# Performance work log

Hardware: AMD Instinct MI355X
Metric: run time of the kernel (lower is better)

Reference implementation:

```python
import jax, jax.numpy as jnp
import numpy as np

N_NODES = 50000
N_RAND_EDGES = 800000
NEG_SLOPE = 0.2


def setup_inputs() -> dict:
    key = jax.random.key(0)
    ks = jax.random.split(key, 10)
    src_r = jax.random.randint(ks[0], (N_RAND_EDGES,), 0, N_NODES, dtype=jnp.int32)
    dst_r = jax.random.randint(ks[1], (N_RAND_EDGES,), 0, N_NODES, dtype=jnp.int32)
    loops = jnp.arange(N_NODES, dtype=jnp.int32)
    src = jnp.concatenate([src_r, loops])  # [E] with self-loops -> no empty softmax segment
    dst = jnp.concatenate([dst_r, loops])
    return {
        "x": jax.random.normal(ks[2], (N_NODES, 256), dtype=jnp.float32),
        "src": src,
        "dst": dst,
        "W0": jax.random.normal(ks[3], (256, 4 * 64), dtype=jnp.float32) * 0.05,
        "al0": jax.random.normal(ks[4], (4, 64), dtype=jnp.float32) * 0.05,
        "ar0": jax.random.normal(ks[5], (4, 64), dtype=jnp.float32) * 0.05,
        "W1": jax.random.normal(ks[6], (256, 1 * 32), dtype=jnp.float32) * 0.05,
        "al1": jax.random.normal(ks[7], (1, 32), dtype=jnp.float32) * 0.05,
        "ar1": jax.random.normal(ks[8], (1, 32), dtype=jnp.float32) * 0.05,
        "Wres": jax.random.normal(ks[9], (256, 32), dtype=jnp.float32) * 0.05,
    }


def gat_conv(x, src, dst, W, al, ar, Wres, activation):
    """DGL-style GATConv. x: [N, F]; W: [F, H*D]; al/ar: [H, D]."""
    N = x.shape[0]
    H, D = al.shape
    feat = (x @ W).reshape(N, H, D)                       # [N,H,D]
    el = jnp.sum(feat * al, axis=-1)                      # [N,H]
    er = jnp.sum(feat * ar, axis=-1)                      # [N,H]
    e = jax.nn.leaky_relu(el[src] + er[dst], NEG_SLOPE)   # [E,H]
    # edge softmax over incoming edges of each dst node
    emax = jax.ops.segment_max(e, dst, num_segments=N)    # [N,H]
    ex = jnp.exp(e - emax[dst])
    denom = jax.ops.segment_sum(ex, dst, num_segments=N)  # [N,H]
    alpha = ex / denom[dst]                               # [E,H]
    msg = feat[src] * alpha[:, :, None]                   # [E,H,D]
    out = jax.ops.segment_sum(msg, dst, num_segments=N)   # [N,H,D]
    if Wres is not None:
        out = out + (x @ Wres).reshape(N, -1, D)          # residual (broadcast over heads)
    if activation is not None:
        out = activation(out)
    return out


def reference(x, src, dst, W0, al0, ar0, W1, al1, ar1, Wres):
    N = x.shape[0]
    h = gat_conv(x, src, dst, W0, al0, ar0, None, jax.nn.elu)  # [N,4,64]
    h = h.reshape(N, -1)                                       # flatten(1) -> [N,256]
    out = gat_conv(h, src, dst, W1, al1, ar1, Wres, None)      # [N,1,32]
    logits = out.mean(axis=1)                                  # [N,32]
    return logits
```

## Files before the change

kernel.cpp:

```cpp
#include <hip/hip_runtime.h>
#include <math.h>

#define NEG_SLOPE 0.2f

typedef __attribute__((ext_vector_type(8))) short short8;
typedef __attribute__((ext_vector_type(4))) float f32x4;
typedef unsigned int uintx2 __attribute__((ext_vector_type(2)));
typedef unsigned int uintx4 __attribute__((ext_vector_type(4)));

__device__ __forceinline__ float leaky(float x) { return x > 0.f ? x : NEG_SLOPE * x; }
__device__ __forceinline__ unsigned enc(float f) {
    unsigned u = __float_as_uint(f);
    return (u & 0x80000000u) ? ~u : (u | 0x80000000u);
}
__device__ __forceinline__ float dec(unsigned e) {
    return (e & 0x80000000u) ? __uint_as_float(e ^ 0x80000000u) : __uint_as_float(~e);
}
__device__ __forceinline__ unsigned bf16u(float f) {
    unsigned u = __float_as_uint(f);
    return (u + 0x7fffu + ((u >> 16) & 1u)) >> 16;
}
__device__ __forceinline__ float blo(unsigned u) { return __uint_as_float(u << 16); }
__device__ __forceinline__ float bhi(unsigned u) { return __uint_as_float(u & 0xffff0000u); }

__global__ __launch_bounds__(256) void prep_kernel(const float* __restrict__ W0,
                                                   unsigned short* __restrict__ W0P,
                                                   const float* __restrict__ W1,
                                                   const float* __restrict__ Wres,
                                                   unsigned short* __restrict__ Bt1,
                                                   const int* __restrict__ dst,
                                                   int* __restrict__ deg, int E) {
    int b = blockIdx.x, tid = threadIdx.x;
    if (b < 256) {
        int n = b, k = tid;
        W0P[(k >> 5) * 8192 + n * 32 + (k & 31)] = (unsigned short)bf16u(W0[k * 256 + n]);
    } else if (b < 320) {
        int n = b - 256, k = tid;
        float v = (n < 32) ? W1[k * 32 + n] : Wres[k * 32 + (n - 32)];
        Bt1[n * 256 + k] = (unsigned short)bf16u(v);
    } else {
        int e = (b - 320) * 256 + tid;
        if (e < E) atomicAdd(&deg[dst[e]], 1);
    }
}

__global__ __launch_bounds__(256) void gemm0_all(const float* __restrict__ x,
                                                 const unsigned short* __restrict__ W0P,
                                                 unsigned short* __restrict__ featS,
                                                 float* __restrict__ el0, float* __restrict__ er0,
                                                 const float* __restrict__ al,
                                                 const float* __restrict__ ar,
                                                 unsigned* __restrict__ gmax, int M) {
    __shared__ unsigned short As[64 * 40];
    __shared__ unsigned short Bs[256 * 40];
    __shared__ __align__(16) unsigned short tile[64 * 72];
    __shared__ float sEl[4][64], sEr[4][64];
    const int K = 256;
    int tid = threadIdx.x, lane = tid & 63, wv = tid >> 6;
    int m0 = blockIdx.x * 64;
    int wm = (wv >> 1) * 32, wn = (wv & 1) * 32;
    f32x4 acc[4][2][2] = {};
    int arow = tid >> 2, apart = tid & 3;
    bool avalid = (m0 + arow) < M;
    const float* Ap = x + (size_t)min(m0 + arow, M - 1) * K + apart * 8;
    const float4 z4 = make_float4(0.f, 0.f, 0.f, 0.f);

    uint4 apReg;
    {
        float4 a0 = avalid ? *(const float4*)Ap : z4;
        float4 a1 = avalid ? *(const float4*)(Ap + 4) : z4;
        apReg.x = bf16u(a0.x) | (bf16u(a0.y) << 16);
        apReg.y = bf16u(a0.z) | (bf16u(a0.w) << 16);
        apReg.z = bf16u(a1.x) | (bf16u(a1.y) << 16);
        apReg.w = bf16u(a1.z) | (bf16u(a1.w) << 16);
    }
    uint4 b[4];
#pragma unroll
    for (int p = 0; p < 4; ++p) b[p] = *(const uint4*)(W0P + (p * 256 + tid) * 8);

    for (int k0 = 0; k0 < K; k0 += 32) {
        *(uint4*)&As[arow * 40 + apart * 8] = apReg;
#pragma unroll
        for (int p = 0; p < 4; ++p) {
            int q = p * 256 + tid;
            *(uint4*)&Bs[(q >> 2) * 40 + (q & 3) * 8] = b[p];
        }
        __syncthreads();
        if (k0 + 32 < K) {
            float4 a0 = avalid ? *(const float4*)(Ap + k0 + 32) : z4;
            float4 a1 = avalid ? *(const float4*)(Ap + k0 + 36) : z4;
            apReg.x = bf16u(a0.x) | (bf16u(a0.y) << 16);
            apReg.y = bf16u(a0.z) | (bf16u(a0.w) << 16);
            apReg.z = bf16u(a1.x) | (bf16u(a1.y) << 16);
            apReg.w = bf16u(a1.z) | (bf16u(a1.w) << 16);
            const unsigned short* slab = W0P + ((k0 >> 5) + 1) * 8192;
#pragma unroll
            for (int p = 0; p < 4; ++p) b[p] = *(const uint4*)(slab + (p * 256 + tid) * 8);
        }
        short8 af[2];
#pragma unroll
        for (int i = 0; i < 2; ++i)
            af[i] = *(const short8*)&As[(wm + i * 16 + (lane & 15)) * 40 + (lane >> 4) * 8];
#pragma unroll
        for (int y = 0; y < 4; ++y) {
            short8 bf[2];
#pragma unroll
            for (int j = 0; j < 2; ++j)
                bf[j] = *(const short8*)&Bs[(y * 64 + wn + j * 16 + (lane & 15)) * 40 + (lane >> 4) * 8];
#pragma unroll
            for (int i = 0; i < 2; ++i)
#pragma unroll
                for (int j = 0; j < 2; ++j)
                    acc[y][i][j] = __builtin_amdgcn_mfma_f32_16x16x32_bf16(af[i], bf[j], acc[y][i][j], 0, 0, 0);
        }
        __syncthreads();
    }

    size_t N32 = (size_t)M * 32;
#pragma unroll
    for (int y = 0; y < 4; ++y) {
#pragma unroll
        for (int i = 0; i < 2; ++i)
#pragma unroll
            for (int j = 0; j < 2; ++j)
#pragma unroll
                for (int r = 0; r < 4; ++r)
                    tile[(wm + i * 16 + (lane >> 4) * 4 + r) * 72 + wn + j * 16 + (lane & 15)] =
                        (unsigned short)bf16u(acc[y][i][j][r]);
        __syncthreads();
#pragma unroll
        for (int u = tid; u < 512; u += 256) {
            int ch = u >> 8, node = (u >> 2) & 63, part = u & 3;
            int row = m0 + node;
            if (row < M) {
                uint4 v = *(const uint4*)&tile[node * 72 + ch * 32 + part * 8];
                *(uint4*)&featS[(size_t)(2 * y + ch) * N32 + (size_t)row * 32 + part * 8] = v;
            }
        }
        {
            int row = tid >> 2, qr = tid & 3;
            float pe = 0.f, pr = 0.f;
            for (int k2 = 0; k2 < 16; ++k2) {
                int c = qr * 16 + k2;
                float f = __uint_as_float((unsigned)tile[row * 72 + c] << 16);
                pe += f * al[y * 64 + c];
                pr += f * ar[y * 64 + c];
            }
            pe += __shfl_xor(pe, 1); pe += __shfl_xor(pe, 2);
            pr += __shfl_xor(pr, 1); pr += __shfl_xor(pr, 2);
            if (qr == 0) {
                bool vv = (m0 + row) < M;
                if (vv) {
                    el0[(m0 + row) * 4 + y] = pe;
                    er0[(m0 + row) * 4 + y] = pr;
                }
                sEl[y][row] = vv ? pe : -1e30f;
                sEr[y][row] = vv ? pr : -1e30f;
            }
        }
        __syncthreads();
    }
    {
        float m1 = sEl[wv][lane];
        float m2 = sEr[wv][lane];
#pragma unroll
        for (int o = 1; o <= 32; o <<= 1) {
            m1 = fmaxf(m1, __shfl_xor(m1, o));
            m2 = fmaxf(m2, __shfl_xor(m2, o));
        }
        if (lane == 0) atomicMax(&gmax[wv], enc(m1));
        if (lane == 1) atomicMax(&gmax[4 + wv], enc(m2));
    }
}

__global__ __launch_bounds__(256) void gemm1_fused(const unsigned short* __restrict__ hbS,
                                                   const unsigned short* __restrict__ Bt,
                                                   float* __restrict__ fcat,
                                                   unsigned short* __restrict__ fg16,
                                                   float* __restrict__ el1, float* __restrict__ er1,
                                                   const float* __restrict__ al,
                                                   const float* __restrict__ ar,
                                                   unsigned* __restrict__ gmax, int M) {
    __shared__ unsigned short As[64 * 40];
    __shared__ unsigned short Bs[64 * 40];
    __shared__ __align__(16) float tileF[64 * 68];
    __shared__ float sEl[64], sEr[64];
    const int K = 256;
    int tid = threadIdx.x, lane = tid & 63, wv = tid >> 6;
    int m0 = blockIdx.x * 64;
    int wm = (wv >> 1) * 32, wn = (wv & 1) * 32;
    f32x4 acc[2][2] = {};
    int srow = tid >> 2, scol = (tid & 3) * 8;
    bool avalid = (m0 + srow) < M;
    size_t arow = (size_t)min(m0 + srow, M - 1);
    size_t N32 = (size_t)M * 32;
    const unsigned short* Bp = Bt + (size_t)srow * K + scol;

    for (int k0 = 0; k0 < K; k0 += 32) {
        const unsigned short* Ap = hbS + (size_t)(k0 >> 5) * N32 + arow * 32 + scol;
        uint4 av = avalid ? *(const uint4*)Ap : make_uint4(0, 0, 0, 0);
        float4 bv = *(const float4*)(Bp + k0);
        *(uint4*)&As[srow * 40 + scol] = av;
        *(float4*)&Bs[srow * 40 + scol] = bv;
        __syncthreads();
        short8 af[2], bf[2];
#pragma unroll
        for (int i = 0; i < 2; ++i) {
            af[i] = *(const short8*)&As[(wm + i * 16 + (lane & 15)) * 40 + (lane >> 4) * 8];
            bf[i] = *(const short8*)&Bs[(wn + i * 16 + (lane & 15)) * 40 + (lane >> 4) * 8];
        }
#pragma unroll
        for (int i = 0; i < 2; ++i)
#pragma unroll
            for (int j = 0; j < 2; ++j)
                acc[i][j] = __builtin_amdgcn_mfma_f32_16x16x32_bf16(af[i], bf[j], acc[i][j], 0, 0, 0);
        __syncthreads();
    }
#pragma unroll
    for (int i = 0; i < 2; ++i)
#pragma unroll
        for (int j = 0; j < 2; ++j)
#pragma unroll
            for (int r = 0; r < 4; ++r)
                tileF[(wm + i * 16 + (lane >> 4) * 4 + r) * 68 + wn + j * 16 + (lane & 15)] =
                    acc[i][j][r];
    __syncthreads();
#pragma unroll
    for (int u = tid; u < 1024; u += 256) {
        int node = u >> 4, part = u & 15;
        int row = m0 + node;
        if (row < M)
            *(uint4*)&fcat[(size_t)row * 64 + part * 4] = *(const uint4*)&tileF[node * 68 + part * 4];
    }
#pragma unroll
    for (int u = tid; u < 1024; u += 256) {
        int node = u >> 4, part = u & 15;
        int row = m0 + node;
        if (row < M) {
            float f0 = tileF[node * 68 + part * 2];
            float f1 = tileF[node * 68 + part * 2 + 1];
            ((unsigned*)fg16)[(size_t)row * 16 + part] = bf16u(f0) | (bf16u(f1) << 16);
        }
    }
    {
        int row = tid >> 2, qr = tid & 3;
        float pe = 0.f, pr = 0.f;
        for (int k = 0; k < 8; ++k) {
            int c = qr * 8 + k;
            float f = tileF[row * 68 + c];
            pe += f * al[c];
            pr += f * ar[c];
        }
        pe += __shfl_xor(pe, 1); pe += __shfl_xor(pe, 2);
        pr += __shfl_xor(pr, 1); pr += __shfl_xor(pr, 2);
        if (qr == 0) {
            bool vv = (m0 + row) < M;
            if (vv) {
                el1[m0 + row] = pe;
                er1[m0 + row] = pr;
            }
            sEl[row] = vv ? pe : -1e30f;
            sEr[row] = vv ? pr : -1e30f;
        }
    }
    __syncthreads();
    if (tid < 64) {
        float m = sEl[tid];
#pragma unroll
        for (int o = 1; o <= 32; o <<= 1) m = fmaxf(m, __shfl_xor(m, o));
        if (tid == 0) atomicMax(&gmax[8], enc(m));
    } else if (tid < 128) {
        float m = sEr[tid - 64];
#pragma unroll
        for (int o = 1; o <= 32; o <<= 1) m = fmaxf(m, __shfl_xor(m, o));
        if (tid == 64) atomicMax(&gmax[9], enc(m));
    }
}

__global__ __launch_bounds__(256) void scanA(const int* __restrict__ deg, int* __restrict__ bsum, int N) {
    int i = blockIdx.x * 256 + threadIdx.x;
    int v = (i < N) ? deg[i] : 0;
#pragma unroll
    for (int o = 32; o > 0; o >>= 1) v += __shfl_xor(v, o);
    __shared__ int s[4];
    if ((threadIdx.x & 63) == 0) s[threadIdx.x >> 6] = v;
    __syncthreads();
    if (threadIdx.x == 0) bsum[blockIdx.x] = s[0] + s[1] + s[2] + s[3];
}

__global__ __launch_bounds__(256) void scanB(const int* __restrict__ bsum, int* __restrict__ bpre, int nb) {
    __shared__ int s[256];
    int t = threadIdx.x;
    int v = (t < nb) ? bsum[t] : 0;
    s[t] = v;
    __syncthreads();
    for (int o = 1; o < 256; o <<= 1) {
        int x = (t >= o) ? s[t - o] : 0;
        __syncthreads();
        s[t] += x;
        __syncthreads();
    }
    if (t < nb) bpre[t] = s[t] - v;
}

__global__ __launch_bounds__(256) void scanC(const int* __restrict__ deg, const int* __restrict__ bpre,
                                             int* __restrict__ off, int N) {
    int b = blockIdx.x, t = threadIdx.x;
    int i = b * 256 + t;
    int v = (i < N) ? deg[i] : 0;
    __shared__ int s[256];
    s[t] = v;
    __syncthreads();
    for (int o = 1; o < 256; o <<= 1) {
        int x = (t >= o) ? s[t - o] : 0;
        __syncthreads();
        s[t] += x;
        __syncthreads();
    }
    int incl = s[t];
    int base = bpre[b];
    if (i < N) off[i] = base + incl - v;
    if (i == N - 1) off[N] = base + incl;
}

__global__ void scatter_kernel(const int* __restrict__ src, const int* __restrict__ dst,
                               const int* __restrict__ off, int* __restrict__ cursor,
                               int* __restrict__ csr_src, int E) {
    int e = blockIdx.x * 256 + threadIdx.x;
    if (e < E) {
        int d = dst[e];
        int pos = atomicAdd(&cursor[d], 1);
        csr_src[off[d] + pos] = src[e];
    }
}

__global__ __launch_bounds__(256) void w0norm(const float* __restrict__ el,
                                              const float* __restrict__ er,
                                              const unsigned* __restrict__ gmax,
                                              const int* __restrict__ off,
                                              const int* __restrict__ csr_src,
                                              unsigned* __restrict__ pk0,
                                              float* __restrict__ dinv0, int N, int E) {
    int tid = threadIdx.x, lane = tid & 63, wv = tid >> 6;
    int grp = lane >> 4, j = lane & 15;
    float C0 = leaky(dec(gmax[0]) + dec(gmax[4]));
    float C1 = leaky(dec(gmax[1]) + dec(gmax[5]));
    float C2 = leaky(dec(gmax[2]) + dec(gmax[6]));
    float C3 = leaky(dec(gmax[3]) + dec(gmax[7]));
    int n = blockIdx.x * 16 + wv * 4 + grp;
    if (n >= N) return;
    int base = off[n], deg = off[n + 1] - base;
    float4 ern = *(const float4*)&er[n * 4];
    float d0 = 0.f, d1 = 0.f, d2 = 0.f, d3 = 0.f;
    for (int j0 = 0; j0 < deg; j0 += 16) {
        int jj = j0 + j;
        if (jj < deg) {
            int idx = base + jj;
            int s = csr_src[idx];
            float4 e4 = *(const float4*)&el[s * 4];
            unsigned b0 = bf16u(__expf(leaky(e4.x + ern.x) - C0));
            unsigned b1 = bf16u(__expf(leaky(e4.y + ern.y) - C1));
            unsigned b2 = bf16u(__expf(leaky(e4.z + ern.z) - C2));
            unsigned b3 = bf16u(__expf(leaky(e4.w + ern.w) - C3));
            unsigned sh = (unsigned)s << 16;
            pk0[idx] = sh | b0;
            pk0[E + idx] = sh | b1;
            pk0[2 * E + idx] = sh | b2;
            pk0[3 * E + idx] = sh | b3;
            d0 += __uint_as_float(b0 << 16);
            d1 += __uint_as_float(b1 << 16);
            d2 += __uint_as_float(b2 << 16);
            d3 += __uint_as_float(b3 << 16);
        }
    }
#pragma unroll
    for (int o = 1; o <= 8; o <<= 1) {
        d0 += __shfl_xor(d0, o);
        d1 += __shfl_xor(d1, o);
        d2 += __shfl_xor(d2, o);
        d3 += __shfl_xor(d3, o);
    }
    if (j == 0) {
        float4 iv = make_float4(1.f / d0, 1.f / d1, 1.f / d2, 1.f / d3);
        *(float4*)&dinv0[n * 4] = iv;
    }
}

__global__ __launch_bounds__(256) void w1norm(const float* __restrict__ el,
                                              const float* __restrict__ er,
                                              const unsigned* __restrict__ gmax,
                                              const int* __restrict__ off,
                                              const int* __restrict__ csr_src,
                                              unsigned* __restrict__ pk1,
                                              float* __restrict__ dinv1, int N) {
    int tid = threadIdx.x, lane = tid & 63, wv = tid >> 6;
    float C = leaky(dec(gmax[8]) + dec(gmax[9]));
    int n = blockIdx.x * 4 + wv;
    if (n >= N) return;
    int base = off[n], deg = off[n + 1] - base;
    float ern = er[n];
    float den = 0.f;
    for (int j0 = 0; j0 < deg; j0 += 64) {
        int jj = j0 + lane;
        if (jj < deg) {
            int idx = base + jj;
            int s = csr_src[idx];
            unsigned b = bf16u(__expf(leaky(el[s] + ern) - C));
            pk1[idx] = ((unsigned)s << 16) | b;
            den += __uint_as_float(b << 16);
        }
    }
#pragma unroll
    for (int o = 1; o <= 32; o <<= 1) den += __shfl_xor(den, o);
    if (lane == 0) dinv1[n] = 1.f / den;
}

__global__ __launch_bounds__(256) void agg0_kernel(const unsigned short* __restrict__ featS,
                                                   const unsigned* __restrict__ pk0,
                                                   const float* __restrict__ dinv0,
                                                   const int* __restrict__ off,
                                                   unsigned short* __restrict__ hbS, int N, int E) {
    int tid = threadIdx.x;
    int c = blockIdx.x & 7, h = c >> 1;
    int gblk = blockIdx.x >> 3, G = gridDim.x >> 3;
    int grp = tid >> 2, ld = tid & 3;
    size_t N32 = (size_t)N * 32;
    const char* Fb = (const char*)(featS + (size_t)c * N32) + ld * 16;
    const unsigned* PH = pk0 + (size_t)h * E;
    for (int n = gblk * 64 + grp; n < N; n += G * 64) {
        int base = off[n], deg = off[n + 1] - base;
        float a0 = 0.f, a1 = 0.f, a2 = 0.f, a3 = 0.f;
        float a4 = 0.f, a5 = 0.f, a6 = 0.f, a7 = 0.f;
        const unsigned* P = PH + base;
        int j = 0;
        for (; j + 4 <= deg; j += 4) {
            unsigned p0 = P[j], p1 = P[j + 1], p2 = P[j + 2], p3 = P[j + 3];
            uintx4 u0 = *(const uintx4*)(Fb + (size_t)(p0 >> 16) * 64);
            uintx4 u1 = *(const uintx4*)(Fb + (size_t)(p1 >> 16) * 64);
            uintx4 u2 = *(const uintx4*)(Fb + (size_t)(p2 >> 16) * 64);
            uintx4 u3 = *(const uintx4*)(Fb + (size_t)(p3 >> 16) * 64);
            float w0 = blo(p0), w1 = blo(p1), w2 = blo(p2), w3 = blo(p3);
            a0 += w0 * blo(u0.x); a1 += w0 * bhi(u0.x);
            a2 += w0 * blo(u0.y); a3 += w0 * bhi(u0.y);
            a4 += w0 * blo(u0.z); a5 += w0 * bhi(u0.z);
            a6 += w0 * blo(u0.w); a7 += w0 * bhi(u0.w);
            a0 += w1 * blo(u1.x); a1 += w1 * bhi(u1.x);
            a2 += w1 * blo(u1.y); a3 += w1 * bhi(u1.y);
            a4 += w1 * blo(u1.z); a5 += w1 * bhi(u1.z);
            a6 += w1 * blo(u1.w); a7 += w1 * bhi(u1.w);
            a0 += w2 * blo(u2.x); a1 += w2 * bhi(u2.x);
            a2 += w2 * blo(u2.y); a3 += w2 * bhi(u2.y);
            a4 += w2 * blo(u2.z); a5 += w2 * bhi(u2.z);
            a6 += w2 * blo(u2.w); a7 += w2 * bhi(u2.w);
            a0 += w3 * blo(u3.x); a1 += w3 * bhi(u3.x);
            a2 += w3 * blo(u3.y); a3 += w3 * bhi(u3.y);
            a4 += w3 * blo(u3.z); a5 += w3 * bhi(u3.z);
            a6 += w3 * blo(u3.w); a7 += w3 * bhi(u3.w);
        }
        for (; j < deg; ++j) {
            unsigned p = P[j];
            float w = blo(p);
            uintx4 u = *(const uintx4*)(Fb + (size_t)(p >> 16) * 64);
            a0 += w * blo(u.x); a1 += w * bhi(u.x);
            a2 += w * blo(u.y); a3 += w * bhi(u.y);
            a4 += w * blo(u.z); a5 += w * bhi(u.z);
            a6 += w * blo(u.w); a7 += w * bhi(u.w);
        }
        float inv = dinv0[n * 4 + h];
        float v0 = a0 * inv, v1 = a1 * inv, v2 = a2 * inv, v3 = a3 * inv;
        float v4 = a4 * inv, v5 = a5 * inv, v6 = a6 * inv, v7 = a7 * inv;
        v0 = v0 > 0.f ? v0 : (__expf(v0) - 1.f);
        v1 = v1 > 0.f ? v1 : (__expf(v1) - 1.f);
        v2 = v2 > 0.f ? v2 : (__expf(v2) - 1.f);
        v3 = v3 > 0.f ? v3 : (__expf(v3) - 1.f);
        v4 = v4 > 0.f ? v4 : (__expf(v4) - 1.f);
        v5 = v5 > 0.f ? v5 : (__expf(v5) - 1.f);
        v6 = v6 > 0.f ? v6 : (__expf(v6) - 1.f);
        v7 = v7 > 0.f ? v7 : (__expf(v7) - 1.f);
        uintx4 o;
        o.x = bf16u(v0) | (bf16u(v1) << 16);
        o.y = bf16u(v2) | (bf16u(v3) << 16);
        o.z = bf16u(v4) | (bf16u(v5) << 16);
        o.w = bf16u(v6) | (bf16u(v7) << 16);
        __builtin_nontemporal_store(o, (uintx4*)&hbS[(size_t)c * N32 + (size_t)n * 32 + ld * 8]);
    }
}

__global__ __launch_bounds__(256) void agg1_kernel(const float* __restrict__ fcat,
                                                   const unsigned short* __restrict__ fg16,
                                                   const unsigned* __restrict__ pk1,
                                                   const float* __restrict__ dinv1,
                                                   const int* __restrict__ off,
                                                   float* __restrict__ out, int N) {
    int tid = threadIdx.x;
    int grp = tid >> 3, ld = tid & 7;
    const char* Fb = (const char*)fg16 + ld * 8;
    for (int n = blockIdx.x * 32 + grp; n < N; n += gridDim.x * 32) {
        int base = off[n], deg = off[n + 1] - base;
        float a0 = 0.f, a1 = 0.f, a2 = 0.f, a3 = 0.f;
        const unsigned* P = pk1 + base;
        int j = 0;
        for (; j + 4 <= deg; j += 4) {
            unsigned p0 = P[j], p1 = P[j + 1], p2 = P[j + 2], p3 = P[j + 3];
            uintx2 u0 = *(const uintx2*)(Fb + (size_t)(p0 >> 16) * 64);
            uintx2 u1 = *(const uintx2*)(Fb + (size_t)(p1 >> 16) * 64);
            uintx2 u2 = *(const uintx2*)(Fb + (size_t)(p2 >> 16) * 64);
            uintx2 u3 = *(const uintx2*)(Fb + (size_t)(p3 >> 16) * 64);
            float w0 = blo(p0), w1 = blo(p1), w2 = blo(p2), w3 = blo(p3);
            a0 += w0 * blo(u0.x); a1 += w0 * bhi(u0.x);
            a2 += w0 * blo(u0.y); a3 += w0 * bhi(u0.y);
            a0 += w1 * blo(u1.x); a1 += w1 * bhi(u1.x);
            a2 += w1 * blo(u1.y); a3 += w1 * bhi(u1.y);
            a0 += w2 * blo(u2.x); a1 += w2 * bhi(u2.x);
            a2 += w2 * blo(u2.y); a3 += w2 * bhi(u2.y);
            a0 += w3 * blo(u3.x); a1 += w3 * bhi(u3.x);
            a2 += w3 * blo(u3.y); a3 += w3 * bhi(u3.y);
        }
        for (; j < deg; ++j) {
            unsigned p = P[j];
            float w = blo(p);
            uintx2 u = *(const uintx2*)(Fb + (size_t)(p >> 16) * 64);
            a0 += w * blo(u.x); a1 += w * bhi(u.x);
            a2 += w * blo(u.y); a3 += w * bhi(u.y);
        }
        float inv = dinv1[n];
        f32x4 res = *(const f32x4*)&fcat[(size_t)n * 64 + 32 + ld * 4];
        f32x4 o;
        o.x = a0 * inv + res.x;
        o.y = a1 * inv + res.y;
        o.z = a2 * inv + res.z;
        o.w = a3 * inv + res.w;
        __builtin_nontemporal_store(o, (f32x4*)&out[(size_t)n * 32 + ld * 4]);
    }
}

extern "C" void kernel_launch(void* const* d_in, const int* in_sizes, int n_in,
                              void* d_out, int out_size, void* d_ws, size_t ws_size,
                              hipStream_t stream) {
    const float* x    = (const float*)d_in[0];
    const int*   src  = (const int*)d_in[1];
    const int*   dst  = (const int*)d_in[2];
    const float* W0   = (const float*)d_in[3];
    const float* al0  = (const float*)d_in[4];
    const float* ar0  = (const float*)d_in[5];
    const float* W1   = (const float*)d_in[6];
    const float* al1  = (const float*)d_in[7];
    const float* ar1  = (const float*)d_in[8];
    const float* Wres = (const float*)d_in[9];
    float* out = (float*)d_out;

    const int N = in_sizes[0] / 256;
    const int E = in_sizes[1];

    unsigned short* hbS   = (unsigned short*)d_ws;
    unsigned short* featS = hbS + (size_t)N * 256;
    unsigned short* W0P   = featS + (size_t)N * 256;
    unsigned short* Bt1   = W0P + 256 * 256;
    unsigned short* fg16  = Bt1 + 64 * 256;
    float* fcat  = (float*)(fg16 + (size_t)N * 32);
    float* el0   = fcat + (size_t)N * 64;
    float* er0   = el0 + (size_t)N * 4;
    float* el1   = er0 + (size_t)N * 4;
    float* er1   = el1 + N;
    float* dinv0 = er1 + N;
    float* dinv1 = dinv0 + (size_t)N * 4;
    unsigned* pk0 = (unsigned*)(dinv1 + N);
    unsigned* pk1 = pk0 + (size_t)E * 4;
    int*   deg    = (int*)(pk1 + E);
    int*   cursor = deg + N;
    unsigned* gmax = (unsigned*)(cursor + N);
    int*   offs  = (int*)(gmax + 16);
    int*   bsum  = offs + N + 1;
    int*   bpre  = bsum + 256;
    int*   csr_src = bpre + 256;

    const int nb = (N + 255) / 256;
    const int eb = (E + 255) / 256;
    const int mb = (N + 63) / 64;

    hipMemsetAsync(deg, 0, (size_t)(2 * N + 16) * sizeof(int), stream);

    prep_kernel<<<320 + eb, 256, 0, stream>>>(W0, W0P, W1, Wres, Bt1, dst, deg, E);

    scanA<<<nb, 256, 0, stream>>>(deg, bsum, N);
    scanB<<<1, 256, 0, stream>>>(bsum, bpre, nb);
    scanC<<<nb, 256, 0, stream>>>(deg, bpre, offs, N);
    scatter_kernel<<<eb, 256, 0, stream>>>(src, dst, offs, cursor, csr_src, E);

    gemm0_all<<<mb, 256, 0, stream>>>(x, W0P, featS, el0, er0, al0, ar0, gmax, N);
    w0norm<<<(N + 15) / 16, 256, 0, stream>>>(el0, er0, gmax, offs, csr_src, pk0, dinv0, N, E);
    {
        int G = (N + 63) / 64;
        agg0_kernel<<<G * 8, 256, 0, stream>>>(featS, pk0, dinv0, offs, hbS, N, E);
    }

    gemm1_fused<<<mb, 256, 0, stream>>>(hbS, Bt1, fcat, fg16, el1, er1, al1, ar1, gmax, N);
    w1norm<<<(N + 3) / 4, 256, 0, stream>>>(el1, er1, gmax, offs, csr_src, pk1, dinv1, N);
    {
        int G = (N + 31) / 32;
        agg1_kernel<<<G, 256, 0, stream>>>(fcat, fg16, pk1, dinv1, offs, out, N);
    }
}
```

Measured before the change: 303.6 us.

## Shrink gemm0 tile to 32 rows, one head per wave, register epilogue

The first-layer GEMM now uses 32-row blocks with each wave owning one attention head's 64 output columns, which doubles the grid to fill more CUs. The el/er dot products and the per-head max are computed directly from MFMA accumulators with lane shuffles instead of a shared-memory pass, and the output tile reuses the B shared buffer, cutting LDS use and barriers. The cost is that each block reloads the full W0 slab for half as many rows, half the threads sit idle while loading A, and featS is stored in narrower 8-byte chunks.

New measurement: 396.1 us (median of 2 runs). +30.5%, slower.

```diff
diff --git a/kernel.cpp b/kernel.cpp
--- a/kernel.cpp
+++ b/kernel.cpp
@@ -51,24 +51,23 @@
                                                  const float* __restrict__ al,
                                                  const float* __restrict__ ar,
                                                  unsigned* __restrict__ gmax, int M) {
-    __shared__ unsigned short As[64 * 40];
+    __shared__ unsigned short As[32 * 40];
     __shared__ unsigned short Bs[256 * 40];
-    __shared__ __align__(16) unsigned short tile[64 * 72];
-    __shared__ float sEl[4][64], sEr[4][64];
+    unsigned short* tile = Bs;
     const int K = 256;
-    int tid = threadIdx.x, lane = tid & 63, wv = tid >> 6;
-    int m0 = blockIdx.x * 64;
-    int wm = (wv >> 1) * 32, wn = (wv & 1) * 32;
-    f32x4 acc[4][2][2] = {};
+    int tid = threadIdx.x, lane = tid & 63, y = tid >> 6;
+    int m0 = blockIdx.x * 32;
+    f32x4 acc[2][4] = {};
+    bool aact = tid < 128;
     int arow = tid >> 2, apart = tid & 3;
-    bool avalid = (m0 + arow) < M;
-    const float* Ap = x + (size_t)min(m0 + arow, M - 1) * K + apart * 8;
+    bool avalid = aact && (m0 + arow) < M;
+    const float* Ap = x + (size_t)min(m0 + (arow & 31), M - 1) * K + apart * 8;
     const float4 z4 = make_float4(0.f, 0.f, 0.f, 0.f);
 
-    uint4 apReg;
-    {
-        float4 a0 = avalid ? *(const float4*)Ap : z4;
-        float4 a1 = avalid ? *(const float4*)(Ap + 4) : z4;
+    uint4 apReg = make_uint4(0, 0, 0, 0);
+    if (avalid) {
+        float4 a0 = *(const float4*)Ap;
+        float4 a1 = *(const float4*)(Ap + 4);
         apReg.x = bf16u(a0.x) | (bf16u(a0.y) << 16);
         apReg.y = bf16u(a0.z) | (bf16u(a0.w) << 16);
         apReg.z = bf16u(a1.x) | (bf16u(a1.y) << 16);
@@ -79,7 +78,7 @@
     for (int p = 0; p < 4; ++p) b[p] = *(const uint4*)(W0P + (p * 256 + tid) * 8);
 
     for (int k0 = 0; k0 < K; k0 += 32) {
-        *(uint4*)&As[arow * 40 + apart * 8] = apReg;
+        if (aact) *(uint4*)&As[arow * 40 + apart * 8] = apReg;
 #pragma unroll
         for (int p = 0; p < 4; ++p) {
             int q = p * 256 + tid;
@@ -87,12 +86,14 @@
         }
         __syncthreads();
         if (k0 + 32 < K) {
-            float4 a0 = avalid ? *(const float4*)(Ap + k0 + 32) : z4;
-            float4 a1 = avalid ? *(const float4*)(Ap + k0 + 36) : z4;
-            apReg.x = bf16u(a0.x) | (bf16u(a0.y) << 16);
-            apReg.y = bf16u(a0.z) | (bf16u(a0.w) << 16);
-            apReg.z = bf16u(a1.x) | (bf16u(a1.y) << 16);
-            apReg.w = bf16u(a1.z) | (bf16u(a1.w) << 16);
+            if (avalid) {
+                float4 a0 = *(const float4*)(Ap + k0 + 32);
+                float4 a1 = *(const float4*)(Ap + k0 + 36);
+                apReg.x = bf16u(a0.x) | (bf16u(a0.y) << 16);
+                apReg.y = bf16u(a0.z) | (bf16u(a0.w) << 16);
+                apReg.z = bf16u(a1.x) | (bf16u(a1.y) << 16);
+                apReg.w = bf16u(a1.z) | (bf16u(a1.w) << 16);
+            }
             const unsigned short* slab = W0P + ((k0 >> 5) + 1) * 8192;
 #pragma unroll
             for (int p = 0; p < 4; ++p) b[p] = *(const uint4*)(slab + (p * 256 + tid) * 8);
@@ -100,76 +101,73 @@
         short8 af[2];
 #pragma unroll
         for (int i = 0; i < 2; ++i)
-            af[i] = *(const short8*)&As[(wm + i * 16 + (lane & 15)) * 40 + (lane >> 4) * 8];
-#pragma unroll
-        for (int y = 0; y < 4; ++y) {
-            short8 bf[2];
-#pragma unroll
-            for (int j = 0; j < 2; ++j)
-                bf[j] = *(const short8*)&Bs[(y * 64 + wn + j * 16 + (lane & 15)) * 40 + (lane >> 4) * 8];
+            af[i] = *(const short8*)&As[(i * 16 + (lane & 15)) * 40 + (lane >> 4) * 8];
+#pragma unroll
+        for (int j = 0; j < 4; ++j) {
+            short8 bf = *(const short8*)&Bs[(y * 64 + j * 16 + (lane & 15)) * 40 + (lane >> 4) * 8];
 #pragma unroll
             for (int i = 0; i < 2; ++i)
-#pragma unroll
-                for (int j = 0; j < 2; ++j)
-                    acc[y][i][j] = __builtin_amdgcn_mfma_f32_16x16x32_bf16(af[i], bf[j], acc[y][i][j], 0, 0, 0);
-        }
-        __syncthreads();
-    }
-
+                acc[i][j] = __builtin_amdgcn_mfma_f32_16x16x32_bf16(af[i], bf, acc[i][j], 0, 0, 0);
+        }
+        __syncthreads();
+    }
+
+    {
+        float alv[4], arv[4];
+#pragma unroll
+        for (int j = 0; j < 4; ++j) {
+            alv[j] = al[y * 64 + j * 16 + (lane & 15)];
+            arv[j] = ar[y * 64 + j * 16 + (lane & 15)];
+        }
+        float mEl = -1e30f, mEr = -1e30f;
+#pragma unroll
+        for (int i = 0; i < 2; ++i)
+#pragma unroll
+            for (int r = 0; r < 4; ++r) {
+                float pe = acc[i][0][r] * alv[0] + acc[i][1][r] * alv[1] +
+                           acc[i][2][r] * alv[2] + acc[i][3][r] * alv[3];
+                float pr = acc[i][0][r] * arv[0] + acc[i][1][r] * arv[1] +
+                           acc[i][2][r] * arv[2] + acc[i][3][r] * arv[3];
+                pe += __shfl_xor(pe, 1); pe += __shfl_xor(pe, 2);
+                pe += __shfl_xor(pe, 4); pe += __shfl_xor(pe, 8);
+                pr += __shfl_xor(pr, 1); pr += __shfl_xor(pr, 2);
+                pr += __shfl_xor(pr, 4); pr += __shfl_xor(pr, 8);
+                int node = i * 16 + (lane >> 4) * 4 + r;
+                if ((lane & 15) == 0 && (m0 + node) < M) {
+                    el0[(m0 + node) * 4 + y] = pe;
+                    er0[(m0 + node) * 4 + y] = pr;
+                    mEl = fmaxf(mEl, pe);
+                    mEr = fmaxf(mEr, pr);
+                }
+            }
+#pragma unroll
+        for (int o = 1; o <= 32; o <<= 1) {
+            mEl = fmaxf(mEl, __shfl_xor(mEl, o));
+            mEr = fmaxf(mEr, __shfl_xor(mEr, o));
+        }
+        if (lane == 0) {
+            atomicMax(&gmax[y], enc(mEl));
+            atomicMax(&gmax[4 + y], enc(mEr));
+        }
+    }
+#pragma unroll
+    for (int i = 0; i < 2; ++i)
+#pragma unroll
+        for (int j = 0; j < 4; ++j)
+#pragma unroll
+            for (int r = 0; r < 4; ++r)
+                tile[(i * 16 + (lane >> 4) * 4 + r) * 264 + y * 64 + j * 16 + (lane & 15)] =
+                    (unsigned short)bf16u(acc[i][j][r]);
+    __syncthreads();
     size_t N32 = (size_t)M * 32;
 #pragma unroll
-    for (int y = 0; y < 4; ++y) {
-#pragma unroll
-        for (int i = 0; i < 2; ++i)
-#pragma unroll
-            for (int j = 0; j < 2; ++j)
-#pragma unroll
-                for (int r = 0; r < 4; ++r)
-                    tile[(wm + i * 16 + (lane >> 4) * 4 + r) * 72 + wn + j * 16 + (lane & 15)] =
-                        (unsigned short)bf16u(acc[y][i][j][r]);
-        __syncthreads();
-#pragma unroll
-        for (int u = tid; u < 512; u += 256) {
-            int ch = u >> 8, node = (u >> 2) & 63, part = u & 3;
-            int row = m0 + node;
-            if (row < M) {
-                uint4 v = *(const uint4*)&tile[node * 72 + ch * 32 + part * 8];
-                *(uint4*)&featS[(size_t)(2 * y + ch) * N32 + (size_t)row * 32 + part * 8] = v;
-            }
-        }
-        {
-            int row = tid >> 2, qr = tid & 3;
-            float pe = 0.f, pr = 0.f;
-            for (int k2 = 0; k2 < 16; ++k2) {
-                int c = qr * 16 + k2;
-                float f = __uint_as_float((unsigned)tile[row * 72 + c] << 16);
-                pe += f * al[y * 64 + c];
-                pr += f * ar[y * 64 + c];
-            }
-            pe += __shfl_xor(pe, 1); pe += __shfl_xor(pe, 2);
-            pr += __shfl_xor(pr, 1); pr += __shfl_xor(pr, 2);
-            if (qr == 0) {
-                bool vv = (m0 + row) < M;
-                if (vv) {
-                    el0[(m0 + row) * 4 + y] = pe;
-                    er0[(m0 + row) * 4 + y] = pr;
-                }
-                sEl[y][row] = vv ? pe : -1e30f;
-                sEr[y][row] = vv ? pr : -1e30f;
-            }
-        }
-        __syncthreads();
-    }
-    {
-        float m1 = sEl[wv][lane];
-        float m2 = sEr[wv][lane];
-#pragma unroll
-        for (int o = 1; o <= 32; o <<= 1) {
-            m1 = fmaxf(m1, __shfl_xor(m1, o));
-            m2 = fmaxf(m2, __shfl_xor(m2, o));
-        }
-        if (lane == 0) atomicMax(&gmax[wv], enc(m1));
-        if (lane == 1) atomicMax(&gmax[4 + wv], enc(m2));
+    for (int u = tid; u < 2048; u += 256) {
+        int ch = u >> 8, node = (u >> 3) & 31, part4 = u & 7;
+        int row = m0 + node;
+        if (row < M) {
+            uintx2 v = *(const uintx2*)&tile[node * 264 + ch * 32 + part4 * 4];
+            *(uintx2*)&featS[(size_t)ch * N32 + (size_t)row * 32 + part4 * 4] = v;
+        }
     }
 }
 
@@ -576,7 +574,6 @@
 
     const int nb = (N + 255) / 256;
     const int eb = (E + 255) / 256;
-    const int mb = (N + 63) / 64;
 
     hipMemsetAsync(deg, 0, (size_t)(2 * N + 16) * sizeof(int), stream);
 
@@ -587,14 +584,14 @@
     scanC<<<nb, 256, 0, stream>>>(deg, bpre, offs, N);
     scatter_kernel<<<eb, 256, 0, stream>>>(src, dst, offs, cursor, csr_src, E);
 
-    gemm0_all<<<mb, 256, 0, stream>>>(x, W0P, featS, el0, er0, al0, ar0, gmax, N);
+    gemm0_all<<<(N + 31) / 32, 256, 0, stream>>>(x, W0P, featS, el0, er0, al0, ar0, gmax, N);
     w0norm<<<(N + 15) / 16, 256, 0, stream>>>(el0, er0, gmax, offs, csr_src, pk0, dinv0, N, E);
     {
         int G = (N + 63) / 64;
         agg0_kernel<<<G * 8, 256, 0, stream>>>(featS, pk0, dinv0, offs, hbS, N, E);
     }
 
-    gemm1_fused<<<mb, 256, 0, stream>>>(hbS, Bt1, fcat, fg16, el1, er1, al1, ar1, gmax, N);
+    gemm1_fused<<<(N + 63) / 64, 256, 0, stream>>>(hbS, Bt1, fcat, fg16, el1, er1, al1, ar1, gmax, N);
     w1norm<<<(N + 3) / 4, 256, 0, stream>>>(el1, er1, gmax, offs, csr_src, pk1, dinv1, N);
     {
         int G = (N + 31) / 32;
```
